# Kernel tuning notes

Measured on AMD Instinct MI355X. Metric: run time of the kernel, lower is better.

The kernel has to match this reference:

```python
import jax, jax.numpy as jnp
import numpy as np

B, T, C, H = 4, 2048, 1024, 16
HS = C // H  # 64
THRESH_INIT = (5 + 1) / 12 * 0.01  # (layer_idx+1)/n_layer * final_token_threshold


def _layernorm(x, w, b, eps=1e-5):
    mu = jnp.mean(x, axis=-1, keepdims=True)
    var = jnp.var(x, axis=-1, keepdims=True)
    return (x - mu) * jax.lax.rsqrt(var + eps) * w + b


def setup_inputs() -> dict:
    key = jax.random.key(0)
    ks = jax.random.split(key, 8)
    s = 0.02
    inp = {
        'x': jax.random.normal(ks[0], (B, T, C), dtype=jnp.float32),
        'attention_mask': jnp.ones((B, T), dtype=jnp.float32),
        'protected_mask': jnp.zeros((B, T), dtype=jnp.float32),
        'ln1_w': jnp.ones((C,), jnp.float32),
        'ln1_b': jnp.zeros((C,), jnp.float32),
        'c_attn_w': jax.random.normal(ks[1], (3 * C, C), jnp.float32) * s,
        'c_attn_b': jnp.zeros((3 * C,), jnp.float32),
        'c_proj_w': jax.random.normal(ks[2], (C, C), jnp.float32) * s,
        'c_proj_b': jnp.zeros((C,), jnp.float32),
        'ln2_w': jnp.ones((C,), jnp.float32),
        'ln2_b': jnp.zeros((C,), jnp.float32),
        'fc_w': jax.random.normal(ks[3], (4 * C, C), jnp.float32) * s,
        'fc_b': jnp.zeros((4 * C,), jnp.float32),
        'fcproj_w': jax.random.normal(ks[4], (C, 4 * C), jnp.float32) * s,
        'fcproj_b': jnp.zeros((C,), jnp.float32),
        'threshold': jnp.asarray(THRESH_INIT, jnp.float32),
    }
    return inp


def reference(x, attention_mask, protected_mask, ln1_w, ln1_b, c_attn_w, c_attn_b,
              c_proj_w, c_proj_b, ln2_w, ln2_b, fc_w, fc_b, fcproj_w, fcproj_b, threshold):
    b, t, c = x.shape
    # --- attention with importance scores ---
    h = _layernorm(x, ln1_w, ln1_b)
    qkv = h @ c_attn_w.T + c_attn_b                      # (B,T,3C)
    q, k, v = jnp.split(qkv, 3, axis=-1)
    q = q.reshape(b, t, H, HS).transpose(0, 2, 1, 3)     # (B,H,T,hs)
    k = k.reshape(b, t, H, HS).transpose(0, 2, 1, 3)
    v = v.reshape(b, t, H, HS).transpose(0, 2, 1, 3)
    att = jnp.einsum('bhqd,bhkd->bhqk', q, k) / np.sqrt(HS)
    causal = jnp.tril(jnp.ones((t, t), dtype=bool))      # (T,T)
    att = jnp.where(causal[None, None], att, -jnp.inf)
    att = jnp.where(attention_mask[:, None, None, :] != 0, att, -jnp.inf)
    att = jax.nn.softmax(att, axis=-1)                   # (B,H,T,T)
    y = jnp.einsum('bhqk,bhkd->bhqd', att, v)
    y = y.transpose(0, 2, 1, 3).reshape(b, t, c)
    y = y @ c_proj_w.T + c_proj_b
    importance = att.mean(axis=1).mean(axis=1)           # (B,T): mean over heads, then queries
    # --- pruning ---
    x = x + y
    pruning_mask = (importance >= threshold).astype(x.dtype)  # hard mode
    pruning_mask = jnp.where(protected_mask > 0, jnp.ones_like(pruning_mask), pruning_mask)
    combined_mask = attention_mask * pruning_mask
    x = x * combined_mask[..., None]
    # --- MLP ---
    m = _layernorm(x, ln2_w, ln2_b)
    m = jax.nn.gelu(m @ fc_w.T + fc_b, approximate=False)
    x = x + (m @ fcproj_w.T + fcproj_b)
    pruning_loss = jnp.asarray(0.0, x.dtype)  # hard mode / lambda=0
    return (x, combined_mask, pruning_loss)
```

## Files before the change

kernel.cpp:

```cpp
#include <hip/hip_runtime.h>
#include <math.h>

#define B_ 4
#define T_ 2048
#define C_ 1024
#define H_ 16
#define NROWS (B_*T_)

typedef short s8v  __attribute__((ext_vector_type(8)));
typedef float f4v  __attribute__((ext_vector_type(4)));
typedef unsigned short u16v4 __attribute__((ext_vector_type(4)));

#define QSCALE 0.1803368801111f

static __device__ __forceinline__ unsigned short f2bf(float x) {
    unsigned u = __float_as_uint(x);
    unsigned r = u + 0x7fffu + ((u >> 16) & 1u);
    return (unsigned short)(r >> 16);
}

static __device__ __forceinline__ float fexp2(float x) {
    return __builtin_amdgcn_exp2f(x);
}

static __device__ __forceinline__ void gload_lds16(const void* g, void* l) {
    __builtin_amdgcn_global_load_lds(
        (const __attribute__((address_space(1))) void*)g,
        (__attribute__((address_space(3))) void*)l, 16, 0, 0);
}

__global__ __launch_bounds__(256) void ln_bf16(const float* __restrict__ x,
        const float* __restrict__ w, const float* __restrict__ b,
        unsigned short* __restrict__ out, const int* __restrict__ flag)
{
    if (flag && flag[0] == 0) return;
    int row = blockIdx.x;
    int tid = threadIdx.x;
    const float4* xr = (const float4*)(x + (size_t)row * C_);
    float4 v = xr[tid];
    float s  = v.x + v.y + v.z + v.w;
    float ss = v.x*v.x + v.y*v.y + v.z*v.z + v.w*v.w;
    #pragma unroll
    for (int off = 32; off > 0; off >>= 1) {
        s  += __shfl_down(s,  off, 64);
        ss += __shfl_down(ss, off, 64);
    }
    __shared__ float rs[4], rss[4];
    __shared__ float smu, srstd;
    int wave = tid >> 6, lane = tid & 63;
    if (lane == 0) { rs[wave] = s; rss[wave] = ss; }
    __syncthreads();
    if (tid == 0) {
        float S  = rs[0]+rs[1]+rs[2]+rs[3];
        float SS = rss[0]+rss[1]+rss[2]+rss[3];
        float mu = S * (1.0f/C_);
        float var = SS * (1.0f/C_) - mu*mu;
        smu = mu; srstd = rsqrtf(var + 1e-5f);
    }
    __syncthreads();
    float mu = smu, rstd = srstd;
    float4 wv = ((const float4*)w)[tid];
    float4 bv = ((const float4*)b)[tid];
    u16v4 o;
    o.x = f2bf((v.x-mu)*rstd*wv.x + bv.x);
    o.y = f2bf((v.y-mu)*rstd*wv.y + bv.y);
    o.z = f2bf((v.z-mu)*rstd*wv.z + bv.z);
    o.w = f2bf((v.w-mu)*rstd*wv.w + bv.w);
    *(u16v4*)(out + (size_t)row * C_ + tid*4) = o;
}

__global__ __launch_bounds__(256) void cvt_bf16(const float* __restrict__ in,
        unsigned short* __restrict__ out, int n4, const int* __restrict__ flag)
{
    if (flag && flag[0] == 0) return;
    int i = blockIdx.x * 256 + threadIdx.x;
    if (i < n4) {
        float4 v = ((const float4*)in)[i];
        u16v4 o = { f2bf(v.x), f2bf(v.y), f2bf(v.z), f2bf(v.w) };
        *(u16v4*)(out + (size_t)i*4) = o;
    }
}

__global__ __launch_bounds__(256) void cvt3_bf16(
        const float* __restrict__ cprojw, const float* __restrict__ fcw,
        const float* __restrict__ fcpw,
        unsigned short* __restrict__ wproj, unsigned short* __restrict__ wfc,
        unsigned short* __restrict__ wfcp, const int* __restrict__ flag)
{
    if (flag[0] == 0) return;
    int i = blockIdx.x * 256 + threadIdx.x;
    const int n1 = C_*C_/4;
    const int n2 = n1 + C_*C_;
    const float* src; unsigned short* dst; int j;
    if (i < n1)      { src = cprojw; dst = wproj; j = i; }
    else if (i < n2) { src = fcw;    dst = wfc;   j = i - n1; }
    else             { src = fcpw;   dst = wfcp;  j = i - n2; }
    float4 v = ((const float4*)src)[j];
    u16v4 o = { f2bf(v.x), f2bf(v.y), f2bf(v.z), f2bf(v.w) };
    *(u16v4*)(dst + (size_t)j*4) = o;
}

__global__ void zero_kernel(float* p, int n) {
    int i = blockIdx.x * 256 + threadIdx.x;
    if (i < n) p[i] = 0.f;
}

template<int EPI>
__global__ __launch_bounds__(256) void gemm_bf16(
    const unsigned short* __restrict__ A,
    const unsigned short* __restrict__ Bw,
    const float* __restrict__ bias,
    const float* __restrict__ res,
    float* __restrict__ Cout, unsigned short* __restrict__ Cbf,
    int K, int lda, int ldb, int ldc, int ncoff,
    const float* __restrict__ cmv,
    unsigned short* __restrict__ qh, unsigned short* __restrict__ kh,
    unsigned short* __restrict__ vh, const int* __restrict__ flag)
{
    if (flag && flag[0] == 0) return;
    __shared__ unsigned short As[128*64];
    __shared__ unsigned short Bs[128*64];
    int tid = threadIdx.x;
    int w = tid >> 6, lane = tid & 63, quad = lane >> 4, l16 = lane & 15;
    int wr = w >> 1, wc = w & 1;
    int m0 = blockIdx.y * 128, n0 = blockIdx.x * 128;

    size_t offA[4], offB[4];
    #pragma unroll
    for (int j = 0; j < 4; j++) {
        int ci = j*256 + tid;
        int mr = ci >> 3, kcs = ci & 7;
        int kc = kcs ^ (mr & 7);
        offA[j] = (size_t)(m0 + mr) * lda + kc*8;
        offB[j] = (size_t)(n0 + mr) * ldb + kc*8;
    }

    f4v acc[4][4];
    #pragma unroll
    for (int i = 0; i < 4; i++)
        #pragma unroll
        for (int j = 0; j < 4; j++) { acc[i][j][0]=0.f; acc[i][j][1]=0.f; acc[i][j][2]=0.f; acc[i][j][3]=0.f; }

    for (int k0 = 0; k0 < K; k0 += 64) {
        __syncthreads();
        #pragma unroll
        for (int j = 0; j < 4; j++) {
            gload_lds16(A  + offA[j] + k0, &As[(j*256 + (w<<6))*8]);
            gload_lds16(Bw + offB[j] + k0, &Bs[(j*256 + (w<<6))*8]);
        }
        __syncthreads();
        #pragma unroll
        for (int c = 0; c < 2; c++) {
            s8v af[4], bf[4];
            int sw = ((c<<2) + quad) ^ (l16 & 7);
            #pragma unroll
            for (int i = 0; i < 4; i++) {
                int mr = wr*64 + i*16 + l16;
                af[i] = *(const s8v*)&As[mr*64 + sw*8];
                int nr = wc*64 + i*16 + l16;
                bf[i] = *(const s8v*)&Bs[nr*64 + sw*8];
            }
            #pragma unroll
            for (int i = 0; i < 4; i++)
                #pragma unroll
                for (int j = 0; j < 4; j++)
                    acc[i][j] = __builtin_amdgcn_mfma_f32_16x16x32_bf16(af[i], bf[j], acc[i][j], 0, 0, 0);
        }
    }

    #pragma unroll
    for (int j = 0; j < 4; j++) {
        int ncol = n0 + wc*64 + j*16 + l16;
        float bv = bias ? bias[ncol] : 0.f;
        int hh = 0, dd = 0;
        bool qsec = false;
        unsigned short* basep = nullptr;
        if (EPI == 3) {
            int ncolg = ncol + ncoff;
            int sec = ncolg >> 10;
            int hn = ncolg & 1023;
            hh = hn >> 6; dd = hn & 63;
            basep = (sec == 0) ? qh : (sec == 1) ? kh : vh;
            qsec = (sec == 0);
        }
        #pragma unroll
        for (int i = 0; i < 4; i++) {
            #pragma unroll
            for (int reg = 0; reg < 4; reg++) {
                int m = m0 + wr*64 + i*16 + quad*4 + reg;
                float v = acc[i][j][reg] + bv;
                if (EPI == 1) {
                    v = 0.5f * v * (1.0f + erff(v * 0.70710678118654752f));
                    Cbf[(size_t)m*ldc + ncol] = f2bf(v);
                } else if (EPI == 2) {
                    Cout[(size_t)m*ldc + ncol] = v + res[(size_t)m*ldc + ncol];
                } else if (EPI == 3) {
                    if (qsec) v *= QSCALE;
                    int bb = m >> 11, t = m & 2047;
                    basep[(((size_t)(bb*H_ + hh))*T_ + t)*64 + dd] = f2bf(v);
                } else if (EPI == 4) {
                    Cout[(size_t)m*ldc + ncol] = (res[(size_t)m*ldc + ncol] + v) * cmv[m];
                }
            }
        }
    }
}

__global__ __launch_bounds__(256) void attn_rowsum(
    const unsigned short* __restrict__ qh, const unsigned short* __restrict__ kh,
    const float* __restrict__ amask, float* __restrict__ linvbuf)
{
    __shared__ float msk01[2048];
    __shared__ float lred[4][64];

    int tid = threadIdx.x;
    int w = tid >> 6, lane = tid & 63, quad = lane >> 4, l16 = lane & 15;
    int qt = 31 - (blockIdx.x >> 6);
    int bh = blockIdx.x & 63;
    int b  = bh >> 4;
    int q0 = qt * 64;
    int ntiles = qt + 1;

    const unsigned short* qp = qh + (size_t)bh*T_*64;
    const unsigned short* kp = kh + (size_t)bh*T_*64;
    const float* amp = amask + b*T_;

    for (int i = tid; i < ntiles*64; i += 256)
        msk01[i] = (amp[i] != 0.f) ? 1.f : 0.f;
    __syncthreads();

    s8v aQ[4][2];
    #pragma unroll
    for (int qf = 0; qf < 4; qf++) {
        int row = q0 + qf*16 + l16;
        aQ[qf][0] = *(const s8v*)(qp + (size_t)row*64 + quad*8);
        aQ[qf][1] = *(const s8v*)(qp + (size_t)row*64 + 32 + quad*8);
    }

    float lrow[4][4];
    #pragma unroll
    for (int qf = 0; qf < 4; qf++)
        #pragma unroll
        for (int reg = 0; reg < 4; reg++) lrow[qf][reg] = 0.f;

    for (int it = w; it < ntiles; it += 4) {
        int k0 = it * 64;
        s8v bk[2][4];
        #pragma unroll
        for (int c = 0; c < 2; c++)
            #pragma unroll
            for (int nt = 0; nt < 4; nt++)
                bk[c][nt] = *(const s8v*)(kp + (size_t)(k0 + nt*16 + l16)*64 + c*32 + quad*8);
        float mk[4];
        #pragma unroll
        for (int nt = 0; nt < 4; nt++) mk[nt] = msk01[k0 + nt*16 + l16];
        bool allm = __all(mk[0] != 0.f && mk[1] != 0.f && mk[2] != 0.f && mk[3] != 0.f);

        #pragma unroll
        for (int qf = 0; qf < 4; qf++) {
            f4v acc[4];
            #pragma unroll
            for (int nt = 0; nt < 4; nt++) { acc[nt][0]=0.f; acc[nt][1]=0.f; acc[nt][2]=0.f; acc[nt][3]=0.f; }
            #pragma unroll
            for (int c = 0; c < 2; c++)
                #pragma unroll
                for (int nt = 0; nt < 4; nt++)
                    acc[nt] = __builtin_amdgcn_mfma_f32_16x16x32_bf16(aQ[qf][c], bk[c][nt], acc[nt], 0, 0, 0);
            if (it < qt && allm) {
                #pragma unroll
                for (int nt = 0; nt < 4; nt++)
                    #pragma unroll
                    for (int reg = 0; reg < 4; reg++)
                        lrow[qf][reg] += fexp2(acc[nt][reg]);
            } else if (it < qt) {
                #pragma unroll
                for (int nt = 0; nt < 4; nt++)
                    #pragma unroll
                    for (int reg = 0; reg < 4; reg++)
                        lrow[qf][reg] += fexp2(acc[nt][reg]) * mk[nt];
            } else {
                #pragma unroll
                for (int nt = 0; nt < 4; nt++) {
                    int kg = k0 + nt*16 + l16;
                    #pragma unroll
                    for (int reg = 0; reg < 4; reg++) {
                        float me = (kg <= q0 + qf*16 + quad*4 + reg) ? mk[nt] : 0.f;
                        lrow[qf][reg] += fexp2(acc[nt][reg]) * me;
                    }
                }
            }
        }
    }

    #pragma unroll
    for (int qf = 0; qf < 4; qf++)
        #pragma unroll
        for (int reg = 0; reg < 4; reg++) {
            float v = lrow[qf][reg];
            v += __shfl_xor(v, 1); v += __shfl_xor(v, 2);
            v += __shfl_xor(v, 4); v += __shfl_xor(v, 8);
            lrow[qf][reg] = v;
        }
    if (l16 == 0) {
        #pragma unroll
        for (int qf = 0; qf < 4; qf++)
            #pragma unroll
            for (int reg = 0; reg < 4; reg++)
                lred[w][qf*16 + quad*4 + reg] = lrow[qf][reg];
    }
    __syncthreads();
    if (tid < 64) {
        float t = lred[0][tid] + lred[1][tid] + lred[2][tid] + lred[3][tid];
        linvbuf[(size_t)bh*T_ + q0 + tid] = (t > 0.f) ? 1.0f / t : 0.f;
    }
}

__global__ __launch_bounds__(256) void attn_colsum(
    const unsigned short* __restrict__ qh, const unsigned short* __restrict__ kh,
    const float* __restrict__ amask, const float* __restrict__ linvbuf,
    float* __restrict__ imp)
{
    __shared__ float cred[4][64];

    int tid = threadIdx.x;
    int w = tid >> 6, lane = tid & 63, quad = lane >> 4, l16 = lane & 15;
    int kc = blockIdx.x >> 6;
    int bh = blockIdx.x & 63;
    int b  = bh >> 4;
    int k0 = kc * 64;

    const unsigned short* qp = qh + (size_t)bh*T_*64;
    const unsigned short* kp = kh + (size_t)bh*T_*64;
    const float* lp = linvbuf + (size_t)bh*T_;

    s8v bk[2][4];
    float mk[4];
    #pragma unroll
    for (int nt = 0; nt < 4; nt++) {
        int key = k0 + nt*16 + l16;
        bk[0][nt] = *(const s8v*)(kp + (size_t)key*64 + quad*8);
        bk[1][nt] = *(const s8v*)(kp + (size_t)key*64 + 32 + quad*8);
        mk[nt] = amask[b*T_ + key];
    }

    float cs[4] = {0.f, 0.f, 0.f, 0.f};

    for (int qt = kc + w; qt < 32; qt += 4) {
        int q0 = qt * 64;
        #pragma unroll
        for (int qf = 0; qf < 4; qf++) {
            int row = q0 + qf*16 + l16;
            s8v a0 = *(const s8v*)(qp + (size_t)row*64 + quad*8);
            s8v a1 = *(const s8v*)(qp + (size_t)row*64 + 32 + quad*8);
            float4 linv4 = *(const float4*)(lp + q0 + qf*16 + quad*4);
            f4v acc[4];
            #pragma unroll
            for (int nt = 0; nt < 4; nt++) { acc[nt][0]=0.f; acc[nt][1]=0.f; acc[nt][2]=0.f; acc[nt][3]=0.f; }
            #pragma unroll
            for (int nt = 0; nt < 4; nt++) {
                acc[nt] = __builtin_amdgcn_mfma_f32_16x16x32_bf16(a0, bk[0][nt], acc[nt], 0, 0, 0);
                acc[nt] = __builtin_amdgcn_mfma_f32_16x16x32_bf16(a1, bk[1][nt], acc[nt], 0, 0, 0);
            }
            float lv[4] = { linv4.x, linv4.y, linv4.z, linv4.w };
            if (qt > kc) {
                #pragma unroll
                for (int nt = 0; nt < 4; nt++)
                    #pragma unroll
                    for (int reg = 0; reg < 4; reg++)
                        cs[nt] += fexp2(acc[nt][reg]) * lv[reg];
            } else {
                #pragma unroll
                for (int nt = 0; nt < 4; nt++) {
                    int kg = k0 + nt*16 + l16;
                    #pragma unroll
                    for (int reg = 0; reg < 4; reg++) {
                        float me = (kg <= q0 + qf*16 + quad*4 + reg) ? 1.f : 0.f;
                        cs[nt] += fexp2(acc[nt][reg]) * lv[reg] * me;
                    }
                }
            }
        }
    }

    #pragma unroll
    for (int nt = 0; nt < 4; nt++) {
        float v = cs[nt] * mk[nt];
        v += __shfl_xor(v, 16);
        v += __shfl_xor(v, 32);
        if (quad == 0) cred[w][nt*16 + l16] = v;
    }
    __syncthreads();
    if (tid < 64)
        atomicAdd(&imp[b*T_ + k0 + tid],
                  cred[0][tid] + cred[1][tid] + cred[2][tid] + cred[3][tid]);
}

__global__ __launch_bounds__(256) void mask_finalize(
    const float* __restrict__ imp, const float* __restrict__ amask,
    const float* __restrict__ prot, const float* __restrict__ thr,
    float* __restrict__ mask_out, float* __restrict__ loss_out,
    int* __restrict__ nsurv)
{
    int i = blockIdx.x * 256 + threadIdx.x;
    float impv = imp[i] * (1.0f / (float)(H_ * T_));
    float pm = (impv >= thr[0]) ? 1.f : 0.f;
    if (prot[i] > 0.f) pm = 1.f;
    float cm = amask[i] * pm;
    mask_out[i] = cm;
    if (i == 0) loss_out[0] = 0.f;
    unsigned long long bal = __ballot(cm != 0.f);
    int cnt = __popcll(bal);
    __shared__ int bs;
    if (threadIdx.x == 0) bs = 0;
    __syncthreads();
    if ((threadIdx.x & 63) == 0 && cnt) atomicAdd(&bs, cnt);
    __syncthreads();
    if (threadIdx.x == 0 && bs) atomicAdd(nsurv, bs);
}

__global__ __launch_bounds__(256) void attn_full(
    const unsigned short* __restrict__ qh, const unsigned short* __restrict__ kh,
    const unsigned short* __restrict__ vh, const float* __restrict__ amask,
    unsigned short* __restrict__ y, const int* __restrict__ flag)
{
    if (flag[0] == 0) return;
    __shared__ unsigned short Ks[64][72];
    __shared__ unsigned short Vt[64][72];
    __shared__ unsigned short Ps[4][16][72];
    __shared__ float mks[64];

    int tid = threadIdx.x;
    int w = tid >> 6, lane = tid & 63, quad = lane >> 4, l16 = lane & 15;
    int nqt = T_ / 64;
    int qt = blockIdx.x % nqt;
    int bh = blockIdx.x / nqt;
    int b = bh >> 4, h = bh & 15;
    int q0 = qt * 64;

    const unsigned short* qp = qh + (size_t)bh * T_ * 64;
    const unsigned short* kp = kh + (size_t)bh * T_ * 64;
    const unsigned short* vp = vh + (size_t)bh * T_ * 64;

    int qrow = q0 + 16*w + l16;
    s8v aQ0 = *(const s8v*)(qp + (size_t)qrow*64 + quad*8);
    s8v aQ1 = *(const s8v*)(qp + (size_t)qrow*64 + 32 + quad*8);

    int qwmax = q0 + 16*w + 15;
    int ntiles = qt + 1;
    int qg = q0 + 16*w + quad*4;

    float lrow[4] = {0.f, 0.f, 0.f, 0.f};
    for (int it = 0; it < ntiles; ++it) {
        int k0 = it * 64;
        __syncthreads();
        for (int cid = tid; cid < 512; cid += 256) {
            int row = cid >> 3, ch = cid & 7;
            *(s8v*)&Ks[row][ch*8] = *(const s8v*)(kp + (size_t)(k0+row)*64 + ch*8);
        }
        if (tid < 64) mks[tid] = amask[b*T_ + k0 + tid];
        __syncthreads();
        if (k0 > qwmax) continue;
        f4v accS[4];
        #pragma unroll
        for (int nt = 0; nt < 4; nt++) { accS[nt][0]=0.f; accS[nt][1]=0.f; accS[nt][2]=0.f; accS[nt][3]=0.f; }
        #pragma unroll
        for (int nt = 0; nt < 4; nt++) {
            s8v b0 = *(const s8v*)&Ks[nt*16 + l16][quad*8];
            s8v b1 = *(const s8v*)&Ks[nt*16 + l16][32 + quad*8];
            accS[nt] = __builtin_amdgcn_mfma_f32_16x16x32_bf16(aQ0, b0, accS[nt], 0, 0, 0);
            accS[nt] = __builtin_amdgcn_mfma_f32_16x16x32_bf16(aQ1, b1, accS[nt], 0, 0, 0);
        }
        #pragma unroll
        for (int nt = 0; nt < 4; nt++) {
            int kg = k0 + nt*16 + l16;
            float mkv = mks[nt*16 + l16];
            #pragma unroll
            for (int reg = 0; reg < 4; reg++) {
                bool val = (kg <= qg + reg) && (mkv != 0.f);
                float e = fexp2(accS[nt][reg]);
                lrow[reg] += val ? e : 0.f;
            }
        }
    }
    float linv[4];
    #pragma unroll
    for (int reg = 0; reg < 4; reg++) {
        float v = lrow[reg];
        v += __shfl_xor(v, 1); v += __shfl_xor(v, 2);
        v += __shfl_xor(v, 4); v += __shfl_xor(v, 8);
        linv[reg] = (v > 0.f) ? 1.0f / v : 0.f;
    }

    f4v accO[4];
    #pragma unroll
    for (int nt = 0; nt < 4; nt++) { accO[nt][0]=0.f; accO[nt][1]=0.f; accO[nt][2]=0.f; accO[nt][3]=0.f; }

    for (int it = 0; it < ntiles; ++it) {
        int k0 = it * 64;
        __syncthreads();
        for (int cid = tid; cid < 512; cid += 256) {
            int row = cid >> 3, ch = cid & 7;
            s8v kv = *(const s8v*)(kp + (size_t)(k0+row)*64 + ch*8);
            *(s8v*)&Ks[row][ch*8] = kv;
            s8v vv = *(const s8v*)(vp + (size_t)(k0+row)*64 + ch*8);
            #pragma unroll
            for (int j = 0; j < 8; j++) Vt[ch*8 + j][row] = (unsigned short)vv[j];
        }
        if (tid < 64) mks[tid] = amask[b*T_ + k0 + tid];
        __syncthreads();
        if (k0 > qwmax) continue;
        f4v accS[4];
        #pragma unroll
        for (int nt = 0; nt < 4; nt++) { accS[nt][0]=0.f; accS[nt][1]=0.f; accS[nt][2]=0.f; accS[nt][3]=0.f; }
        #pragma unroll
        for (int nt = 0; nt < 4; nt++) {
            s8v b0 = *(const s8v*)&Ks[nt*16 + l16][quad*8];
            s8v b1 = *(const s8v*)&Ks[nt*16 + l16][32 + quad*8];
            accS[nt] = __builtin_amdgcn_mfma_f32_16x16x32_bf16(aQ0, b0, accS[nt], 0, 0, 0);
            accS[nt] = __builtin_amdgcn_mfma_f32_16x16x32_bf16(aQ1, b1, accS[nt], 0, 0, 0);
        }
        #pragma unroll
        for (int nt = 0; nt < 4; nt++) {
            int kg = k0 + nt*16 + l16;
            float mkv = mks[nt*16 + l16];
            #pragma unroll
            for (int reg = 0; reg < 4; reg++) {
                bool val = (kg <= qg + reg) && (mkv != 0.f);
                float p = val ? fexp2(accS[nt][reg]) * linv[reg] : 0.f;
                Ps[w][quad*4 + reg][nt*16 + l16] = f2bf(p);
            }
        }
        s8v aP0 = *(const s8v*)&Ps[w][l16][quad*8];
        s8v aP1 = *(const s8v*)&Ps[w][l16][32 + quad*8];
        #pragma unroll
        for (int nt = 0; nt < 4; nt++) {
            s8v bv0 = *(const s8v*)&Vt[nt*16 + l16][quad*8];
            s8v bv1 = *(const s8v*)&Vt[nt*16 + l16][32 + quad*8];
            accO[nt] = __builtin_amdgcn_mfma_f32_16x16x32_bf16(aP0, bv0, accO[nt], 0, 0, 0);
            accO[nt] = __builtin_amdgcn_mfma_f32_16x16x32_bf16(aP1, bv1, accO[nt], 0, 0, 0);
        }
    }
    #pragma unroll
    for (int nt = 0; nt < 4; nt++) {
        #pragma unroll
        for (int reg = 0; reg < 4; reg++) {
            int q = q0 + 16*w + quad*4 + reg;
            y[((size_t)(b*T_ + q))*C_ + h*64 + nt*16 + l16] = f2bf(accO[nt][reg]);
        }
    }
}

__global__ __launch_bounds__(256) void ap_fc(const int* __restrict__ nsurv,
        const float* __restrict__ ln2b, const float* __restrict__ fcw,
        const float* __restrict__ fcb, float* __restrict__ abuf)
{
    if (nsurv[0] != 0) return;
    int j = blockIdx.x * 4 + (threadIdx.x >> 6);
    int lane = threadIdx.x & 63;
    const float* wr = fcw + (size_t)j * C_;
    float s = 0.f;
    for (int k = lane; k < C_; k += 64) s += ln2b[k] * wr[k];
    #pragma unroll
    for (int off = 32; off > 0; off >>= 1) s += __shfl_down(s, off, 64);
    if (lane == 0) {
        float v = fcb[j] + s;
        abuf[j] = 0.5f * v * (1.0f + erff(v * 0.70710678118654752f));
    }
}

__global__ __launch_bounds__(256) void ap_fcp(const int* __restrict__ nsurv,
        const float* __restrict__ abuf, const float* __restrict__ fcpw,
        const float* __restrict__ fcpb, float* __restrict__ rowbuf)
{
    if (nsurv[0] != 0) return;
    int c = blockIdx.x * 4 + (threadIdx.x >> 6);
    int lane = threadIdx.x & 63;
    const float* wr = fcpw + (size_t)c * (4*C_);
    float s = 0.f;
    for (int k = lane; k < 4*C_; k += 64) s += abuf[k] * wr[k];
    #pragma unroll
    for (int off = 32; off > 0; off >>= 1) s += __shfl_down(s, off, 64);
    if (lane == 0) rowbuf[c] = fcpb[c] + s;
}

__global__ __launch_bounds__(256) void ap_bcast(const int* __restrict__ nsurv,
        const float* __restrict__ rowbuf, float* __restrict__ out_x)
{
    if (nsurv[0] != 0) return;
    int r = blockIdx.x;
    float4 v = ((const float4*)rowbuf)[threadIdx.x];
    ((float4*)(out_x + (size_t)r * C_))[threadIdx.x] = v;
}

extern "C" void kernel_launch(void* const* d_in, const int* in_sizes, int n_in,
                              void* d_out, int out_size, void* d_ws, size_t ws_size,
                              hipStream_t stream) {
    const float* x       = (const float*)d_in[0];
    const float* amask   = (const float*)d_in[1];
    const float* prot    = (const float*)d_in[2];
    const float* ln1w    = (const float*)d_in[3];
    const float* ln1b    = (const float*)d_in[4];
    const float* cattn_w = (const float*)d_in[5];
    const float* cattn_b = (const float*)d_in[6];
    const float* cproj_w = (const float*)d_in[7];
    const float* cproj_b = (const float*)d_in[8];
    const float* ln2w    = (const float*)d_in[9];
    const float* ln2b    = (const float*)d_in[10];
    const float* fcw     = (const float*)d_in[11];
    const float* fcb     = (const float*)d_in[12];
    const float* fcpw    = (const float*)d_in[13];
    const float* fcpb    = (const float*)d_in[14];
    const float* thr     = (const float*)d_in[15];

    unsigned short* wqkv  = (unsigned short*)d_ws;
    unsigned short* wproj = wqkv  + (size_t)3*C_*C_;
    unsigned short* wfc   = wproj + (size_t)C_*C_;
    unsigned short* wfcp  = wfc   + (size_t)4*C_*C_;
    unsigned short* hbuf  = wfcp  + (size_t)4*C_*C_;
    unsigned short* qh    = hbuf  + (size_t)NROWS*C_;
    unsigned short* kh    = qh    + (size_t)NROWS*C_;
    unsigned short* vh    = kh    + (size_t)NROWS*C_;
    unsigned short* cbuf  = qh;
    float* imp    = (float*)(vh + (size_t)NROWS*C_);
    int*   nsurv  = (int*)(imp + NROWS);
    float* abuf   = (float*)(nsurv + 4);
    float* rowbuf = abuf + 4*C_;
    float* linvbuf = rowbuf + C_;

    float* out_x    = (float*)d_out;
    float* out_mask = out_x + (size_t)NROWS*C_;
    float* out_loss = out_mask + NROWS;

    hipLaunchKernelGGL(zero_kernel, dim3((NROWS+8+255)/256), dim3(256), 0, stream,
                       imp, NROWS + 4);
    hipLaunchKernelGGL(cvt_bf16, dim3(3*C_*C_/4/256), dim3(256), 0, stream,
                       cattn_w, wqkv, 3*C_*C_/4, nullptr);
    hipLaunchKernelGGL(ln_bf16, dim3(NROWS), dim3(256), 0, stream, x, ln1w, ln1b, hbuf, nullptr);
    hipLaunchKernelGGL((gemm_bf16<3>), dim3(2048/128, NROWS/128), dim3(256), 0, stream,
                       hbuf, wqkv, cattn_b, nullptr, nullptr, nullptr,
                       C_, C_, C_, 0, 0, nullptr, qh, kh, vh, nullptr);
    hipLaunchKernelGGL(attn_rowsum, dim3(64*32), dim3(256), 0, stream,
                       qh, kh, amask, linvbuf);
    hipLaunchKernelGGL(attn_colsum, dim3(64*32), dim3(256), 0, stream,
                       qh, kh, amask, linvbuf, imp);
    hipLaunchKernelGGL(mask_finalize, dim3(NROWS/256), dim3(256), 0, stream,
                       imp, amask, prot, thr, out_mask, out_loss, nsurv);

    hipLaunchKernelGGL(cvt3_bf16, dim3(9*C_*C_/4/256), dim3(256), 0, stream,
                       cproj_w, fcw, fcpw, wproj, wfc, wfcp, nsurv);
    hipLaunchKernelGGL((gemm_bf16<3>), dim3(1024/128, NROWS/128), dim3(256), 0, stream,
                       hbuf, wqkv + (size_t)2048*C_, cattn_b + 2048, nullptr, nullptr, nullptr,
                       C_, C_, C_, 0, 2048, nullptr, qh, kh, vh, nsurv);
    hipLaunchKernelGGL(attn_full, dim3(B_*H_*(T_/64)), dim3(256), 0, stream,
                       qh, kh, vh, amask, hbuf, nsurv);
    hipLaunchKernelGGL((gemm_bf16<4>), dim3(C_/128, NROWS/128), dim3(256), 0, stream,
                       hbuf, wproj, cproj_b, x, out_x, nullptr,
                       C_, C_, C_, C_, 0, out_mask, nullptr, nullptr, nullptr, nsurv);
    hipLaunchKernelGGL(ln_bf16, dim3(NROWS), dim3(256), 0, stream, out_x, ln2w, ln2b, hbuf, nsurv);
    for (int j = 0; j < 2; j++) {
        hipLaunchKernelGGL((gemm_bf16<1>), dim3(2048/128, NROWS/128), dim3(256), 0, stream,
                           hbuf, wfc + (size_t)j*2048*C_, fcb + j*2048, nullptr, nullptr, cbuf,
                           C_, C_, C_, 2048, 0, nullptr, nullptr, nullptr, nullptr, nsurv);
        hipLaunchKernelGGL((gemm_bf16<2>), dim3(C_/128, NROWS/128), dim3(256), 0, stream,
                           cbuf, wfcp + (size_t)j*2048, (j == 0) ? fcpb : nullptr, out_x, out_x, nullptr,
                           2048, 2048, 4*C_, C_, 0, nullptr, nullptr, nullptr, nullptr, nsurv);
    }

    hipLaunchKernelGGL(ap_fc,    dim3(4*C_/4), dim3(256), 0, stream, nsurv, ln2b, fcw, fcb, abuf);
    hipLaunchKernelGGL(ap_fcp,   dim3(C_/4),   dim3(256), 0, stream, nsurv, abuf, fcpw, fcpb, rowbuf);
    hipLaunchKernelGGL(ap_bcast, dim3(NROWS),  dim3(256), 0, stream, nsurv, rowbuf, out_x);
}
```

Baseline: 348.2 us.

## Fuse prep kernels and use grid-stride persistent grids for flag-gated kernels

Merges zeroing, the QKV weight bf16 conversion and the first layernorm into one prep kernel. Converts the GEMM, attention, layernorm, weight-conversion and broadcast kernels to grid-stride loops launched with fixed 512-block grids, so kernels that exit early on the survivor flag launch far fewer blocks. Also vectorises the all-pruned fallback dot products with float4 loads. The cost is a less tuned block-to-tile mapping when the full path does run, plus extra barriers in the looped layernorm.

```diff
diff --git a/kernel.cpp b/kernel.cpp
--- a/kernel.cpp
+++ b/kernel.cpp
@@ -29,13 +29,23 @@
         (__attribute__((address_space(3))) void*)l, 16, 0, 0);
 }
 
-__global__ __launch_bounds__(256) void ln_bf16(const float* __restrict__ x,
-        const float* __restrict__ w, const float* __restrict__ b,
-        unsigned short* __restrict__ out, const int* __restrict__ flag)
-{
-    if (flag && flag[0] == 0) return;
+__global__ __launch_bounds__(256) void prep_kernel(
+        const float* __restrict__ x, const float* __restrict__ w,
+        const float* __restrict__ b, unsigned short* __restrict__ out,
+        const float* __restrict__ wsrc, unsigned short* __restrict__ wdst,
+        float* __restrict__ imp, int* __restrict__ nsurv)
+{
     int row = blockIdx.x;
     int tid = threadIdx.x;
+    int widx = row * 96 + tid;
+    if (tid < 96) {
+        float4 v = ((const float4*)wsrc)[widx];
+        u16v4 o = { f2bf(v.x), f2bf(v.y), f2bf(v.z), f2bf(v.w) };
+        *(u16v4*)(wdst + (size_t)widx*4) = o;
+    }
+    if (row < 32) imp[row*256 + tid] = 0.f;
+    if (row == 32 && tid < 8) nsurv[tid] = 0;
+
     const float4* xr = (const float4*)(x + (size_t)row * C_);
     float4 v = xr[tid];
     float s  = v.x + v.y + v.z + v.w;
@@ -69,15 +79,45 @@
     *(u16v4*)(out + (size_t)row * C_ + tid*4) = o;
 }
 
-__global__ __launch_bounds__(256) void cvt_bf16(const float* __restrict__ in,
-        unsigned short* __restrict__ out, int n4, const int* __restrict__ flag)
+__global__ __launch_bounds__(256) void ln_bf16(const float* __restrict__ x,
+        const float* __restrict__ w, const float* __restrict__ b,
+        unsigned short* __restrict__ out, const int* __restrict__ flag, int nrows)
 {
     if (flag && flag[0] == 0) return;
-    int i = blockIdx.x * 256 + threadIdx.x;
-    if (i < n4) {
-        float4 v = ((const float4*)in)[i];
-        u16v4 o = { f2bf(v.x), f2bf(v.y), f2bf(v.z), f2bf(v.w) };
-        *(u16v4*)(out + (size_t)i*4) = o;
+    int tid = threadIdx.x;
+    __shared__ float rs[4], rss[4];
+    __shared__ float smu, srstd;
+    int wave = tid >> 6, lane = tid & 63;
+    for (int row = blockIdx.x; row < nrows; row += gridDim.x) {
+        const float4* xr = (const float4*)(x + (size_t)row * C_);
+        float4 v = xr[tid];
+        float s  = v.x + v.y + v.z + v.w;
+        float ss = v.x*v.x + v.y*v.y + v.z*v.z + v.w*v.w;
+        #pragma unroll
+        for (int off = 32; off > 0; off >>= 1) {
+            s  += __shfl_down(s,  off, 64);
+            ss += __shfl_down(ss, off, 64);
+        }
+        if (lane == 0) { rs[wave] = s; rss[wave] = ss; }
+        __syncthreads();
+        if (tid == 0) {
+            float S  = rs[0]+rs[1]+rs[2]+rs[3];
+            float SS = rss[0]+rss[1]+rss[2]+rss[3];
+            float mu = S * (1.0f/C_);
+            float var = SS * (1.0f/C_) - mu*mu;
+            smu = mu; srstd = rsqrtf(var + 1e-5f);
+        }
+        __syncthreads();
+        float mu = smu, rstd = srstd;
+        float4 wv = ((const float4*)w)[tid];
+        float4 bv = ((const float4*)b)[tid];
+        u16v4 o;
+        o.x = f2bf((v.x-mu)*rstd*wv.x + bv.x);
+        o.y = f2bf((v.y-mu)*rstd*wv.y + bv.y);
+        o.z = f2bf((v.z-mu)*rstd*wv.z + bv.z);
+        o.w = f2bf((v.w-mu)*rstd*wv.w + bv.w);
+        *(u16v4*)(out + (size_t)row * C_ + tid*4) = o;
+        __syncthreads();
     }
 }
 
@@ -88,21 +128,18 @@
         unsigned short* __restrict__ wfcp, const int* __restrict__ flag)
 {
     if (flag[0] == 0) return;
-    int i = blockIdx.x * 256 + threadIdx.x;
+    const int total = 9*C_*C_/4;
     const int n1 = C_*C_/4;
     const int n2 = n1 + C_*C_;
-    const float* src; unsigned short* dst; int j;
-    if (i < n1)      { src = cprojw; dst = wproj; j = i; }
-    else if (i < n2) { src = fcw;    dst = wfc;   j = i - n1; }
-    else             { src = fcpw;   dst = wfcp;  j = i - n2; }
-    float4 v = ((const float4*)src)[j];
-    u16v4 o = { f2bf(v.x), f2bf(v.y), f2bf(v.z), f2bf(v.w) };
-    *(u16v4*)(dst + (size_t)j*4) = o;
-}
-
-__global__ void zero_kernel(float* p, int n) {
-    int i = blockIdx.x * 256 + threadIdx.x;
-    if (i < n) p[i] = 0.f;
+    for (int i = blockIdx.x * 256 + threadIdx.x; i < total; i += gridDim.x * 256) {
+        const float* src; unsigned short* dst; int j;
+        if (i < n1)      { src = cprojw; dst = wproj; j = i; }
+        else if (i < n2) { src = fcw;    dst = wfc;   j = i - n1; }
+        else             { src = fcpw;   dst = wfcp;  j = i - n2; }
+        float4 v = ((const float4*)src)[j];
+        u16v4 o = { f2bf(v.x), f2bf(v.y), f2bf(v.z), f2bf(v.w) };
+        *(u16v4*)(dst + (size_t)j*4) = o;
+    }
 }
 
 template<int EPI>
@@ -115,7 +152,8 @@
     int K, int lda, int ldb, int ldc, int ncoff,
     const float* __restrict__ cmv,
     unsigned short* __restrict__ qh, unsigned short* __restrict__ kh,
-    unsigned short* __restrict__ vh, const int* __restrict__ flag)
+    unsigned short* __restrict__ vh, const int* __restrict__ flag,
+    int nbx, int nby)
 {
     if (flag && flag[0] == 0) return;
     __shared__ unsigned short As[128*64];
@@ -123,83 +161,91 @@
     int tid = threadIdx.x;
     int w = tid >> 6, lane = tid & 63, quad = lane >> 4, l16 = lane & 15;
     int wr = w >> 1, wc = w & 1;
-    int m0 = blockIdx.y * 128, n0 = blockIdx.x * 128;
-
-    size_t offA[4], offB[4];
-    #pragma unroll
-    for (int j = 0; j < 4; j++) {
-        int ci = j*256 + tid;
-        int mr = ci >> 3, kcs = ci & 7;
-        int kc = kcs ^ (mr & 7);
-        offA[j] = (size_t)(m0 + mr) * lda + kc*8;
-        offB[j] = (size_t)(n0 + mr) * ldb + kc*8;
-    }
-
-    f4v acc[4][4];
-    #pragma unroll
-    for (int i = 0; i < 4; i++)
-        #pragma unroll
-        for (int j = 0; j < 4; j++) { acc[i][j][0]=0.f; acc[i][j][1]=0.f; acc[i][j][2]=0.f; acc[i][j][3]=0.f; }
-
-    for (int k0 = 0; k0 < K; k0 += 64) {
-        __syncthreads();
+
+    int nvb = nbx * nby;
+    int vb0 = blockIdx.y * gridDim.x + blockIdx.x;
+    int vstride = gridDim.x * gridDim.y;
+
+    for (int vb = vb0; vb < nvb; vb += vstride) {
+        int n0 = (vb % nbx) * 128;
+        int m0 = (vb / nbx) * 128;
+
+        size_t offA[4], offB[4];
         #pragma unroll
         for (int j = 0; j < 4; j++) {
-            gload_lds16(A  + offA[j] + k0, &As[(j*256 + (w<<6))*8]);
-            gload_lds16(Bw + offB[j] + k0, &Bs[(j*256 + (w<<6))*8]);
-        }
-        __syncthreads();
-        #pragma unroll
-        for (int c = 0; c < 2; c++) {
-            s8v af[4], bf[4];
-            int sw = ((c<<2) + quad) ^ (l16 & 7);
+            int ci = j*256 + tid;
+            int mr = ci >> 3, kcs = ci & 7;
+            int kc = kcs ^ (mr & 7);
+            offA[j] = (size_t)(m0 + mr) * lda + kc*8;
+            offB[j] = (size_t)(n0 + mr) * ldb + kc*8;
+        }
+
+        f4v acc[4][4];
+        #pragma unroll
+        for (int i = 0; i < 4; i++)
+            #pragma unroll
+            for (int j = 0; j < 4; j++) { acc[i][j][0]=0.f; acc[i][j][1]=0.f; acc[i][j][2]=0.f; acc[i][j][3]=0.f; }
+
+        for (int k0 = 0; k0 < K; k0 += 64) {
+            __syncthreads();
+            #pragma unroll
+            for (int j = 0; j < 4; j++) {
+                gload_lds16(A  + offA[j] + k0, &As[(j*256 + (w<<6))*8]);
+                gload_lds16(Bw + offB[j] + k0, &Bs[(j*256 + (w<<6))*8]);
+            }
+            __syncthreads();
+            #pragma unroll
+            for (int c = 0; c < 2; c++) {
+                s8v af[4], bf[4];
+                int sw = ((c<<2) + quad) ^ (l16 & 7);
+                #pragma unroll
+                for (int i = 0; i < 4; i++) {
+                    int mr = wr*64 + i*16 + l16;
+                    af[i] = *(const s8v*)&As[mr*64 + sw*8];
+                    int nr = wc*64 + i*16 + l16;
+                    bf[i] = *(const s8v*)&Bs[nr*64 + sw*8];
+                }
+                #pragma unroll
+                for (int i = 0; i < 4; i++)
+                    #pragma unroll
+                    for (int j = 0; j < 4; j++)
+                        acc[i][j] = __builtin_amdgcn_mfma_f32_16x16x32_bf16(af[i], bf[j], acc[i][j], 0, 0, 0);
+            }
+        }
+
+        #pragma unroll
+        for (int j = 0; j < 4; j++) {
+            int ncol = n0 + wc*64 + j*16 + l16;
+            float bv = bias ? bias[ncol] : 0.f;
+            int hh = 0, dd = 0;
+            bool qsec = false;
+            unsigned short* basep = nullptr;
+            if (EPI == 3) {
+                int ncolg = ncol + ncoff;
+                int sec = ncolg >> 10;
+                int hn = ncolg & 1023;
+                hh = hn >> 6; dd = hn & 63;
+                basep = (sec == 0) ? qh : (sec == 1) ? kh : vh;
+                qsec = (sec == 0);
+            }
             #pragma unroll
             for (int i = 0; i < 4; i++) {
-                int mr = wr*64 + i*16 + l16;
-                af[i] = *(const s8v*)&As[mr*64 + sw*8];
-                int nr = wc*64 + i*16 + l16;
-                bf[i] = *(const s8v*)&Bs[nr*64 + sw*8];
-            }
-            #pragma unroll
-            for (int i = 0; i < 4; i++)
-                #pragma unroll
-                for (int j = 0; j < 4; j++)
-                    acc[i][j] = __builtin_amdgcn_mfma_f32_16x16x32_bf16(af[i], bf[j], acc[i][j], 0, 0, 0);
-        }
-    }
-
-    #pragma unroll
-    for (int j = 0; j < 4; j++) {
-        int ncol = n0 + wc*64 + j*16 + l16;
-        float bv = bias ? bias[ncol] : 0.f;
-        int hh = 0, dd = 0;
-        bool qsec = false;
-        unsigned short* basep = nullptr;
-        if (EPI == 3) {
-            int ncolg = ncol + ncoff;
-            int sec = ncolg >> 10;
-            int hn = ncolg & 1023;
-            hh = hn >> 6; dd = hn & 63;
-            basep = (sec == 0) ? qh : (sec == 1) ? kh : vh;
-            qsec = (sec == 0);
-        }
-        #pragma unroll
-        for (int i = 0; i < 4; i++) {
-            #pragma unroll
-            for (int reg = 0; reg < 4; reg++) {
-                int m = m0 + wr*64 + i*16 + quad*4 + reg;
-                float v = acc[i][j][reg] + bv;
-                if (EPI == 1) {
-                    v = 0.5f * v * (1.0f + erff(v * 0.70710678118654752f));
-                    Cbf[(size_t)m*ldc + ncol] = f2bf(v);
-                } else if (EPI == 2) {
-                    Cout[(size_t)m*ldc + ncol] = v + res[(size_t)m*ldc + ncol];
-                } else if (EPI == 3) {
-                    if (qsec) v *= QSCALE;
-                    int bb = m >> 11, t = m & 2047;
-                    basep[(((size_t)(bb*H_ + hh))*T_ + t)*64 + dd] = f2bf(v);
-                } else if (EPI == 4) {
-                    Cout[(size_t)m*ldc + ncol] = (res[(size_t)m*ldc + ncol] + v) * cmv[m];
+                #pragma unroll
+                for (int reg = 0; reg < 4; reg++) {
+                    int m = m0 + wr*64 + i*16 + quad*4 + reg;
+                    float v = acc[i][j][reg] + bv;
+                    if (EPI == 1) {
+                        v = 0.5f * v * (1.0f + erff(v * 0.70710678118654752f));
+                        Cbf[(size_t)m*ldc + ncol] = f2bf(v);
+                    } else if (EPI == 2) {
+                        Cout[(size_t)m*ldc + ncol] = v + res[(size_t)m*ldc + ncol];
+                    } else if (EPI == 3) {
+                        if (qsec) v *= QSCALE;
+                        int bb = m >> 11, t = m & 2047;
+                        basep[(((size_t)(bb*H_ + hh))*T_ + t)*64 + dd] = f2bf(v);
+                    } else if (EPI == 4) {
+                        Cout[(size_t)m*ldc + ncol] = (res[(size_t)m*ldc + ncol] + v) * cmv[m];
+                    }
                 }
             }
         }
@@ -432,121 +478,125 @@
     int tid = threadIdx.x;
     int w = tid >> 6, lane = tid & 63, quad = lane >> 4, l16 = lane & 15;
     int nqt = T_ / 64;
-    int qt = blockIdx.x % nqt;
-    int bh = blockIdx.x / nqt;
-    int b = bh >> 4, h = bh & 15;
-    int q0 = qt * 64;
-
-    const unsigned short* qp = qh + (size_t)bh * T_ * 64;
-    const unsigned short* kp = kh + (size_t)bh * T_ * 64;
-    const unsigned short* vp = vh + (size_t)bh * T_ * 64;
-
-    int qrow = q0 + 16*w + l16;
-    s8v aQ0 = *(const s8v*)(qp + (size_t)qrow*64 + quad*8);
-    s8v aQ1 = *(const s8v*)(qp + (size_t)qrow*64 + 32 + quad*8);
-
-    int qwmax = q0 + 16*w + 15;
-    int ntiles = qt + 1;
-    int qg = q0 + 16*w + quad*4;
-
-    float lrow[4] = {0.f, 0.f, 0.f, 0.f};
-    for (int it = 0; it < ntiles; ++it) {
-        int k0 = it * 64;
+
+    for (int vb = blockIdx.x; vb < B_*H_*nqt; vb += gridDim.x) {
+        int qt = vb % nqt;
+        int bh = vb / nqt;
+        int b = bh >> 4, h = bh & 15;
+        int q0 = qt * 64;
+
+        const unsigned short* qp = qh + (size_t)bh * T_ * 64;
+        const unsigned short* kp = kh + (size_t)bh * T_ * 64;
+        const unsigned short* vp = vh + (size_t)bh * T_ * 64;
+
+        int qrow = q0 + 16*w + l16;
+        s8v aQ0 = *(const s8v*)(qp + (size_t)qrow*64 + quad*8);
+        s8v aQ1 = *(const s8v*)(qp + (size_t)qrow*64 + 32 + quad*8);
+
+        int qwmax = q0 + 16*w + 15;
+        int ntiles = qt + 1;
+        int qg = q0 + 16*w + quad*4;
+
+        float lrow[4] = {0.f, 0.f, 0.f, 0.f};
+        for (int it = 0; it < ntiles; ++it) {
+            int k0 = it * 64;
+            __syncthreads();
+            for (int cid = tid; cid < 512; cid += 256) {
+                int row = cid >> 3, ch = cid & 7;
+                *(s8v*)&Ks[row][ch*8] = *(const s8v*)(kp + (size_t)(k0+row)*64 + ch*8);
+            }
+            if (tid < 64) mks[tid] = amask[b*T_ + k0 + tid];
+            __syncthreads();
+            if (k0 > qwmax) continue;
+            f4v accS[4];
+            #pragma unroll
+            for (int nt = 0; nt < 4; nt++) { accS[nt][0]=0.f; accS[nt][1]=0.f; accS[nt][2]=0.f; accS[nt][3]=0.f; }
+            #pragma unroll
+            for (int nt = 0; nt < 4; nt++) {
+                s8v b0 = *(const s8v*)&Ks[nt*16 + l16][quad*8];
+                s8v b1 = *(const s8v*)&Ks[nt*16 + l16][32 + quad*8];
+                accS[nt] = __builtin_amdgcn_mfma_f32_16x16x32_bf16(aQ0, b0, accS[nt], 0, 0, 0);
+                accS[nt] = __builtin_amdgcn_mfma_f32_16x16x32_bf16(aQ1, b1, accS[nt], 0, 0, 0);
+            }
+            #pragma unroll
+            for (int nt = 0; nt < 4; nt++) {
+                int kg = k0 + nt*16 + l16;
+                float mkv = mks[nt*16 + l16];
+                #pragma unroll
+                for (int reg = 0; reg < 4; reg++) {
+                    bool val = (kg <= qg + reg) && (mkv != 0.f);
+                    float e = fexp2(accS[nt][reg]);
+                    lrow[reg] += val ? e : 0.f;
+                }
+            }
+        }
+        float linv[4];
+        #pragma unroll
+        for (int reg = 0; reg < 4; reg++) {
+            float v = lrow[reg];
+            v += __shfl_xor(v, 1); v += __shfl_xor(v, 2);
+            v += __shfl_xor(v, 4); v += __shfl_xor(v, 8);
+            linv[reg] = (v > 0.f) ? 1.0f / v : 0.f;
+        }
+
+        f4v accO[4];
+        #pragma unroll
+        for (int nt = 0; nt < 4; nt++) { accO[nt][0]=0.f; accO[nt][1]=0.f; accO[nt][2]=0.f; accO[nt][3]=0.f; }
+
+        for (int it = 0; it < ntiles; ++it) {
+            int k0 = it * 64;
+            __syncthreads();
+            for (int cid = tid; cid < 512; cid += 256) {
+                int row = cid >> 3, ch = cid & 7;
+                s8v kv = *(const s8v*)(kp + (size_t)(k0+row)*64 + ch*8);
+                *(s8v*)&Ks[row][ch*8] = kv;
+                s8v vv = *(const s8v*)(vp + (size_t)(k0+row)*64 + ch*8);
+                #pragma unroll
+                for (int j = 0; j < 8; j++) Vt[ch*8 + j][row] = (unsigned short)vv[j];
+            }
+            if (tid < 64) mks[tid] = amask[b*T_ + k0 + tid];
+            __syncthreads();
+            if (k0 > qwmax) continue;
+            f4v accS[4];
+            #pragma unroll
+            for (int nt = 0; nt < 4; nt++) { accS[nt][0]=0.f; accS[nt][1]=0.f; accS[nt][2]=0.f; accS[nt][3]=0.f; }
+            #pragma unroll
+            for (int nt = 0; nt < 4; nt++) {
+                s8v b0 = *(const s8v*)&Ks[nt*16 + l16][quad*8];
+                s8v b1 = *(const s8v*)&Ks[nt*16 + l16][32 + quad*8];
+                accS[nt] = __builtin_amdgcn_mfma_f32_16x16x32_bf16(aQ0, b0, accS[nt], 0, 0, 0);
+                accS[nt] = __builtin_amdgcn_mfma_f32_16x16x32_bf16(aQ1, b1, accS[nt], 0, 0, 0);
+            }
+            #pragma unroll
+            for (int nt = 0; nt < 4; nt++) {
+                int kg = k0 + nt*16 + l16;
+                float mkv = mks[nt*16 + l16];
+                #pragma unroll
+                for (int reg = 0; reg < 4; reg++) {
+                    bool val = (kg <= qg + reg) && (mkv != 0.f);
+                    float p = val ? fexp2(accS[nt][reg]) * linv[reg] : 0.f;
+                    Ps[w][quad*4 + reg][nt*16 + l16] = f2bf(p);
+                }
+            }
+            s8v aP0 = *(const s8v*)&Ps[w][l16][quad*8];
+            s8v aP1 = *(const s8v*)&Ps[w][l16][32 + quad*8];
+            #pragma unroll
+            for (int nt = 0; nt < 4; nt++) {
+                s8v bv0 = *(const s8v*)&Vt[nt*16 + l16][quad*8];
+                s8v bv1 = *(const s8v*)&Vt[nt*16 + l16][32 + quad*8];
+                accO[nt] = __builtin_amdgcn_mfma_f32_16x16x32_bf16(aP0, bv0, accO[nt], 0, 0, 0);
+                accO[nt] = __builtin_amdgcn_mfma_f32_16x16x32_bf16(aP1, bv1, accO[nt], 0, 0, 0);
+            }
+        }
+        #pragma unroll
+        for (int nt = 0; nt < 4; nt++) {
+            #pragma unroll
+            for (int reg = 0; reg < 4; reg++) {
+                int q = q0 + 16*w + quad*4 + reg;
+                y[((size_t)(b*T_ + q))*C_ + h*64 + nt*16 + l16] = f2bf(accO[nt][reg]);
+            }
+        }
         __syncthreads();
-        for (int cid = tid; cid < 512; cid += 256) {
-            int row = cid >> 3, ch = cid & 7;
-            *(s8v*)&Ks[row][ch*8] = *(const s8v*)(kp + (size_t)(k0+row)*64 + ch*8);
-        }
-        if (tid < 64) mks[tid] = amask[b*T_ + k0 + tid];
-        __syncthreads();
-        if (k0 > qwmax) continue;
-        f4v accS[4];
-        #pragma unroll
-        for (int nt = 0; nt < 4; nt++) { accS[nt][0]=0.f; accS[nt][1]=0.f; accS[nt][2]=0.f; accS[nt][3]=0.f; }
-        #pragma unroll
-        for (int nt = 0; nt < 4; nt++) {
-            s8v b0 = *(const s8v*)&Ks[nt*16 + l16][quad*8];
-            s8v b1 = *(const s8v*)&Ks[nt*16 + l16][32 + quad*8];
-            accS[nt] = __builtin_amdgcn_mfma_f32_16x16x32_bf16(aQ0, b0, accS[nt], 0, 0, 0);
-            accS[nt] = __builtin_amdgcn_mfma_f32_16x16x32_bf16(aQ1, b1, accS[nt], 0, 0, 0);
-        }
-        #pragma unroll
-        for (int nt = 0; nt < 4; nt++) {
-            int kg = k0 + nt*16 + l16;
-            float mkv = mks[nt*16 + l16];
-            #pragma unroll
-            for (int reg = 0; reg < 4; reg++) {
-                bool val = (kg <= qg + reg) && (mkv != 0.f);
-                float e = fexp2(accS[nt][reg]);
-                lrow[reg] += val ? e : 0.f;
-            }
-        }
-    }
-    float linv[4];
-    #pragma unroll
-    for (int reg = 0; reg < 4; reg++) {
-        float v = lrow[reg];
-        v += __shfl_xor(v, 1); v += __shfl_xor(v, 2);
-        v += __shfl_xor(v, 4); v += __shfl_xor(v, 8);
-        linv[reg] = (v > 0.f) ? 1.0f / v : 0.f;
-    }
-
-    f4v accO[4];
-    #pragma unroll
-    for (int nt = 0; nt < 4; nt++) { accO[nt][0]=0.f; accO[nt][1]=0.f; accO[nt][2]=0.f; accO[nt][3]=0.f; }
-
-    for (int it = 0; it < ntiles; ++it) {
-        int k0 = it * 64;
-        __syncthreads();
-        for (int cid = tid; cid < 512; cid += 256) {
-            int row = cid >> 3, ch = cid & 7;
-            s8v kv = *(const s8v*)(kp + (size_t)(k0+row)*64 + ch*8);
-            *(s8v*)&Ks[row][ch*8] = kv;
-            s8v vv = *(const s8v*)(vp + (size_t)(k0+row)*64 + ch*8);
-            #pragma unroll
-            for (int j = 0; j < 8; j++) Vt[ch*8 + j][row] = (unsigned short)vv[j];
-        }
-        if (tid < 64) mks[tid] = amask[b*T_ + k0 + tid];
-        __syncthreads();
-        if (k0 > qwmax) continue;
-        f4v accS[4];
-        #pragma unroll
-        for (int nt = 0; nt < 4; nt++) { accS[nt][0]=0.f; accS[nt][1]=0.f; accS[nt][2]=0.f; accS[nt][3]=0.f; }
-        #pragma unroll
-        for (int nt = 0; nt < 4; nt++) {
-            s8v b0 = *(const s8v*)&Ks[nt*16 + l16][quad*8];
-            s8v b1 = *(const s8v*)&Ks[nt*16 + l16][32 + quad*8];
-            accS[nt] = __builtin_amdgcn_mfma_f32_16x16x32_bf16(aQ0, b0, accS[nt], 0, 0, 0);
-            accS[nt] = __builtin_amdgcn_mfma_f32_16x16x32_bf16(aQ1, b1, accS[nt], 0, 0, 0);
-        }
-        #pragma unroll
-        for (int nt = 0; nt < 4; nt++) {
-            int kg = k0 + nt*16 + l16;
-            float mkv = mks[nt*16 + l16];
-            #pragma unroll
-            for (int reg = 0; reg < 4; reg++) {
-                bool val = (kg <= qg + reg) && (mkv != 0.f);
-                float p = val ? fexp2(accS[nt][reg]) * linv[reg] : 0.f;
-                Ps[w][quad*4 + reg][nt*16 + l16] = f2bf(p);
-            }
-        }
-        s8v aP0 = *(const s8v*)&Ps[w][l16][quad*8];
-        s8v aP1 = *(const s8v*)&Ps[w][l16][32 + quad*8];
-        #pragma unroll
-        for (int nt = 0; nt < 4; nt++) {
-            s8v bv0 = *(const s8v*)&Vt[nt*16 + l16][quad*8];
-            s8v bv1 = *(const s8v*)&Vt[nt*16 + l16][32 + quad*8];
-            accO[nt] = __builtin_amdgcn_mfma_f32_16x16x32_bf16(aP0, bv0, accO[nt], 0, 0, 0);
-            accO[nt] = __builtin_amdgcn_mfma_f32_16x16x32_bf16(aP1, bv1, accO[nt], 0, 0, 0);
-        }
-    }
-    #pragma unroll
-    for (int nt = 0; nt < 4; nt++) {
-        #pragma unroll
-        for (int reg = 0; reg < 4; reg++) {
-            int q = q0 + 16*w + quad*4 + reg;
-            y[((size_t)(b*T_ + q))*C_ + h*64 + nt*16 + l16] = f2bf(accO[nt][reg]);
-        }
     }
 }
 
@@ -557,9 +607,15 @@
     if (nsurv[0] != 0) return;
     int j = blockIdx.x * 4 + (threadIdx.x >> 6);
     int lane = threadIdx.x & 63;
-    const float* wr = fcw + (size_t)j * C_;
+    const float4* wr = (const float4*)(fcw + (size_t)j * C_);
+    const float4* bb = (const float4*)ln2b;
     float s = 0.f;
-    for (int k = lane; k < C_; k += 64) s += ln2b[k] * wr[k];
+    #pragma unroll
+    for (int k = 0; k < 4; k++) {
+        float4 a = bb[lane + 64*k];
+        float4 wv = wr[lane + 64*k];
+        s += a.x*wv.x + a.y*wv.y + a.z*wv.z + a.w*wv.w;
+    }
     #pragma unroll
     for (int off = 32; off > 0; off >>= 1) s += __shfl_down(s, off, 64);
     if (lane == 0) {
@@ -575,9 +631,15 @@
     if (nsurv[0] != 0) return;
     int c = blockIdx.x * 4 + (threadIdx.x >> 6);
     int lane = threadIdx.x & 63;
-    const float* wr = fcpw + (size_t)c * (4*C_);
+    const float4* wr = (const float4*)(fcpw + (size_t)c * (4*C_));
+    const float4* ab = (const float4*)abuf;
     float s = 0.f;
-    for (int k = lane; k < 4*C_; k += 64) s += abuf[k] * wr[k];
+    #pragma unroll
+    for (int k = 0; k < 16; k++) {
+        float4 a = ab[lane + 64*k];
+        float4 wv = wr[lane + 64*k];
+        s += a.x*wv.x + a.y*wv.y + a.z*wv.z + a.w*wv.w;
+    }
     #pragma unroll
     for (int off = 32; off > 0; off >>= 1) s += __shfl_down(s, off, 64);
     if (lane == 0) rowbuf[c] = fcpb[c] + s;
@@ -587,9 +649,9 @@
         const float* __restrict__ rowbuf, float* __restrict__ out_x)
 {
     if (nsurv[0] != 0) return;
-    int r = blockIdx.x;
     float4 v = ((const float4*)rowbuf)[threadIdx.x];
-    ((float4*)(out_x + (size_t)r * C_))[threadIdx.x] = v;
+    for (int r = blockIdx.x; r < NROWS; r += gridDim.x)
+        ((float4*)(out_x + (size_t)r * C_))[threadIdx.x] = v;
 }
 
 extern "C" void kernel_launch(void* const* d_in, const int* in_sizes, int n_in,
@@ -623,7 +685,7 @@
     unsigned short* cbuf  = qh;
     float* imp    = (float*)(vh + (size_t)NROWS*C_);
     int*   nsurv  = (int*)(imp + NROWS);
-    float* abuf   = (float*)(nsurv + 4);
+    float* abuf   = (float*)(nsurv + 8);
     float* rowbuf = abuf + 4*C_;
     float* linvbuf = rowbuf + C_;
 
@@ -631,14 +693,11 @@
     float* out_mask = out_x + (size_t)NROWS*C_;
     float* out_loss = out_mask + NROWS;
 
-    hipLaunchKernelGGL(zero_kernel, dim3((NROWS+8+255)/256), dim3(256), 0, stream,
-                       imp, NROWS + 4);
-    hipLaunchKernelGGL(cvt_bf16, dim3(3*C_*C_/4/256), dim3(256), 0, stream,
-                       cattn_w, wqkv, 3*C_*C_/4, nullptr);
-    hipLaunchKernelGGL(ln_bf16, dim3(NROWS), dim3(256), 0, stream, x, ln1w, ln1b, hbuf, nullptr);
-    hipLaunchKernelGGL((gemm_bf16<3>), dim3(2048/128, NROWS/128), dim3(256), 0, stream,
+    hipLaunchKernelGGL(prep_kernel, dim3(NROWS), dim3(256), 0, stream,
+                       x, ln1w, ln1b, hbuf, cattn_w, wqkv, imp, nsurv);
+    hipLaunchKernelGGL((gemm_bf16<3>), dim3(16, 64), dim3(256), 0, stream,
                        hbuf, wqkv, cattn_b, nullptr, nullptr, nullptr,
-                       C_, C_, C_, 0, 0, nullptr, qh, kh, vh, nullptr);
+                       C_, C_, C_, 0, 0, nullptr, qh, kh, vh, nullptr, 16, 64);
     hipLaunchKernelGGL(attn_rowsum, dim3(64*32), dim3(256), 0, stream,
                        qh, kh, amask, linvbuf);
     hipLaunchKernelGGL(attn_colsum, dim3(64*32), dim3(256), 0, stream,
@@ -646,27 +705,28 @@
     hipLaunchKernelGGL(mask_finalize, dim3(NROWS/256), dim3(256), 0, stream,
                        imp, amask, prot, thr, out_mask, out_loss, nsurv);
 
-    hipLaunchKernelGGL(cvt3_bf16, dim3(9*C_*C_/4/256), dim3(256), 0, stream,
+    hipLaunchKernelGGL(cvt3_bf16, dim3(512), dim3(256), 0, stream,
                        cproj_w, fcw, fcpw, wproj, wfc, wfcp, nsurv);
-    hipLaunchKernelGGL((gemm_bf16<3>), dim3(1024/128, NROWS/128), dim3(256), 0, stream,
+    hipLaunchKernelGGL((gemm_bf16<3>), dim3(512), dim3(256), 0, stream,
                        hbuf, wqkv + (size_t)2048*C_, cattn_b + 2048, nullptr, nullptr, nullptr,
-                       C_, C_, C_, 0, 2048, nullptr, qh, kh, vh, nsurv);
-    hipLaunchKernelGGL(attn_full, dim3(B_*H_*(T_/64)), dim3(256), 0, stream,
+                       C_, C_, C_, 0, 2048, nullptr, qh, kh, vh, nsurv, 8, 64);
+    hipLaunchKernelGGL(attn_full, dim3(512), dim3(256), 0, stream,
                        qh, kh, vh, amask, hbuf, nsurv);
-    hipLaunchKernelGGL((gemm_bf16<4>), dim3(C_/128, NROWS/128), dim3(256), 0, stream,
+    hipLaunchKernelGGL((gemm_bf16<4>), dim3(512), dim3(256), 0, stream,
                        hbuf, wproj, cproj_b, x, out_x, nullptr,
-                       C_, C_, C_, C_, 0, out_mask, nullptr, nullptr, nullptr, nsurv);
-    hipLaunchKernelGGL(ln_bf16, dim3(NROWS), dim3(256), 0, stream, out_x, ln2w, ln2b, hbuf, nsurv);
+                       C_, C_, C_, C_, 0, out_mask, nullptr, nullptr, nullptr, nsurv, 8, 64);
+    hipLaunchKernelGGL(ln_bf16, dim3(512), dim3(256), 0, stream,
+                       out_x, ln2w, ln2b, hbuf, nsurv, NROWS);
     for (int j = 0; j < 2; j++) {
-        hipLaunchKernelGGL((gemm_bf16<1>), dim3(2048/128, NROWS/128), dim3(256), 0, stream,
+        hipLaunchKernelGGL((gemm_bf16<1>), dim3(512), dim3(256), 0, stream,
                            hbuf, wfc + (size_t)j*2048*C_, fcb + j*2048, nullptr, nullptr, cbuf,
-                           C_, C_, C_, 2048, 0, nullptr, nullptr, nullptr, nullptr, nsurv);
-        hipLaunchKernelGGL((gemm_bf16<2>), dim3(C_/128, NROWS/128), dim3(256), 0, stream,
+                           C_, C_, C_, 2048, 0, nullptr, nullptr, nullptr, nullptr, nsurv, 16, 64);
+        hipLaunchKernelGGL((gemm_bf16<2>), dim3(512), dim3(256), 0, stream,
                            cbuf, wfcp + (size_t)j*2048, (j == 0) ? fcpb : nullptr, out_x, out_x, nullptr,
-                           2048, 2048, 4*C_, C_, 0, nullptr, nullptr, nullptr, nullptr, nsurv);
+                           2048, 2048, 4*C_, C_, 0, nullptr, nullptr, nullptr, nullptr, nsurv, 8, 64);
     }
 
     hipLaunchKernelGGL(ap_fc,    dim3(4*C_/4), dim3(256), 0, stream, nsurv, ln2b, fcw, fcb, abuf);
     hipLaunchKernelGGL(ap_fcp,   dim3(C_/4),   dim3(256), 0, stream, nsurv, abuf, fcpw, fcpb, rowbuf);
-    hipLaunchKernelGGL(ap_bcast, dim3(NROWS),  dim3(256), 0, stream, nsurv, rowbuf, out_x);
-}
+    hipLaunchKernelGGL(ap_bcast, dim3(512),    dim3(256), 0, stream, nsurv, rowbuf, out_x);
+}
```

After: 311.4 us. 1.12x faster.
